# Kernel optimization log

Measured on AMD Instinct MI355X. Metric: run time of the kernel, lower is better.

The kernel has to match this reference:

```python
import jax, jax.numpy as jnp
import numpy as np

B, S, H, F, E, K = 2, 1024, 1024, 4096, 8, 2
TOPK_RATIO = 0.55
EPS = 1e-8


def _ste(x, q):
    # straight-through estimator: forward = q, backward = identity on x
    return x + jax.lax.stop_gradient(q - x)


def ternary_weight(w):
    # BitNet b1.58 absmean ternarization: W -> clip(round(W/mean|W|), -1, 1) * mean|W|
    s = jnp.maximum(jnp.mean(jnp.abs(w)), EPS)
    q = jnp.clip(jnp.round(w / s), -1.0, 1.0) * s
    return _ste(w, q)


def quant_act_int4(x):
    # per-token symmetric int4 fake-quant (range [-7, 7]) with STE
    s = jnp.maximum(jnp.max(jnp.abs(x), axis=-1, keepdims=True), EPS) / 7.0
    q = jnp.clip(jnp.round(x / s), -7.0, 7.0) * s
    return _ste(x, q)


def quant_act_topk_int8(x, ratio):
    # keep top ceil(ratio*d) values by magnitude per token, then int8 fake-quant
    d = x.shape[-1]
    k = int(np.ceil(ratio * d))
    thresh = jax.lax.top_k(jnp.abs(x), k)[0][..., -1:]
    xm = jnp.where(jnp.abs(x) >= thresh, x, 0.0)
    s = jnp.maximum(jnp.max(jnp.abs(xm), axis=-1, keepdims=True), EPS) / 127.0
    q = jnp.clip(jnp.round(xm / s), -127.0, 127.0) * s
    return _ste(xm, q)


def quant_weight_int8(w):
    # per-tensor absmax int8 fake-quant for the router (Int8Linear) with STE
    s = jnp.maximum(jnp.max(jnp.abs(w)), EPS) / 127.0
    q = jnp.clip(jnp.round(w / s), -127.0, 127.0) * s
    return _ste(w, q)


def setup_inputs() -> dict:
    key = jax.random.key(0)
    ks = jax.random.split(key, 5)
    x = jax.random.normal(ks[0], (B, S, H), jnp.float32)
    w_gate = jax.random.normal(ks[1], (E, F, H), jnp.float32) * 0.02
    w_up = jax.random.normal(ks[2], (E, F, H), jnp.float32) * 0.02
    w_down = jax.random.normal(ks[3], (E, H, F), jnp.float32) * 0.02
    w_router = jax.random.normal(ks[4], (E, H), jnp.float32) * 0.02
    return {"x": x, "w_gate": w_gate, "w_up": w_up, "w_down": w_down, "w_router": w_router}


def reference(x, w_gate, w_up, w_down, w_router):
    T = B * S
    xf = x.reshape(T, H)

    # --- router (Int8Linear, higher precision than ternary) ---
    logits = xf @ quant_weight_int8(w_router).T          # [T, E]
    probs = jax.nn.softmax(logits, axis=-1)
    gates, idx = jax.lax.top_k(probs, K)                  # [T, K]
    gates = gates / jnp.sum(gates, axis=-1, keepdims=True)
    # dense combine weights [T, E]
    comb = jnp.zeros((T, E), x.dtype).at[jnp.arange(T)[:, None], idx].set(gates)

    # --- experts: BitFFN (SwiGLU with ternary weights + quantized activations) ---
    xq = quant_act_int4(xf)                               # shared int4 input quant

    def expert(wg, wu, wd):
        g = xq @ ternary_weight(wg).T                     # [T, F]
        u = xq @ ternary_weight(wu).T                     # [T, F]
        h = jax.nn.silu(g) * u
        hq = quant_act_topk_int8(h, TOPK_RATIO)
        return hq @ ternary_weight(wd).T                  # [T, H]

    expert_out = jax.vmap(expert)(w_gate, w_up, w_down)   # [E, T, H]
    out = jnp.einsum('te,eth->th', comb, expert_out)      # gated combine
    return out.reshape(B, S, H)
```

## Files before the change

### kernel.cpp

```cpp
#include <hip/hip_runtime.h>
#include <cstdint>
#include <cstddef>


#define T_TOK 2048
#define HDIM  1024
#define FDIM  4096
#define NEXP  8
#define FH    (FDIM * HDIM)
#define KTOP  2253
#define EPSF  1e-8f
#define PPAD  4608

typedef int v4i  __attribute__((ext_vector_type(4)));
typedef int v16i __attribute__((ext_vector_type(16)));

__global__ __launch_bounds__(256) void k_wabs_partial(const float* __restrict__ wg,
                                                      const float* __restrict__ wu,
                                                      const float* __restrict__ wd,
                                                      float* __restrict__ partials) {
  int m = blockIdx.x, blk = blockIdx.y, tid = threadIdx.x;
  const float* base = (m < 8) ? (wg + (size_t)m * FH)
                    : (m < 16) ? (wu + (size_t)(m - 8) * FH)
                               : (wd + (size_t)(m - 16) * FH);
  size_t start = (size_t)blk * 65536;
  float s = 0.f;
#pragma unroll 4
  for (int i = 0; i < 64; i++) {
    float4 v = *(const float4*)(base + start + (size_t)i * 1024 + tid * 4);
    s += fabsf(v.x) + fabsf(v.y) + fabsf(v.z) + fabsf(v.w);
  }
  for (int o = 32; o > 0; o >>= 1) s += __shfl_down(s, o);
  __shared__ float lds[4];
  if ((tid & 63) == 0) lds[tid >> 6] = s;
  __syncthreads();
  if (tid == 0) partials[m * 64 + blk] = lds[0] + lds[1] + lds[2] + lds[3];
}

__global__ __launch_bounds__(256) void k_scales(const float* __restrict__ wr,
                                                const float* __restrict__ partials,
                                                float* __restrict__ s_w,
                                                float* __restrict__ wrq) {
  int tid = threadIdx.x;
  __shared__ float lds[4];
  __shared__ float sbc;
  for (int m = 0; m < 24; m++) {
    float v = 0.f;
    if (tid < 64) v = partials[m * 64 + tid];
    for (int o = 32; o > 0; o >>= 1) v += __shfl_down(v, o);
    if ((tid & 63) == 0) lds[tid >> 6] = v;
    __syncthreads();
    if (tid == 0) s_w[m] = fmaxf((lds[0] + lds[1] + lds[2] + lds[3]) / (float)FH, EPSF);
    __syncthreads();
  }
  float mx = 0.f;
  for (int i = tid; i < NEXP * HDIM; i += 256) mx = fmaxf(mx, fabsf(wr[i]));
  for (int o = 32; o > 0; o >>= 1) mx = fmaxf(mx, __shfl_down(mx, o));
  if ((tid & 63) == 0) lds[tid >> 6] = mx;
  __syncthreads();
  if (tid == 0)
    sbc = fmaxf(fmaxf(fmaxf(lds[0], lds[1]), fmaxf(lds[2], lds[3])), EPSF) / 127.0f;
  __syncthreads();
  float s = sbc;
  for (int i = tid; i < NEXP * HDIM; i += 256) {
    float q = fminf(fmaxf(rintf(wr[i] / s), -127.f), 127.f);
    wrq[i] = q * s;
  }
}

template <int KD, int RD>
__global__ __launch_bounds__(256) void k_quant_pack(const float* __restrict__ w,
                                                    signed char* __restrict__ q,
                                                    const float* __restrict__ scales) {
  constexpr int CCH = KD / 32, GR = RD / 32;
  int idx = blockIdx.x * 256 + threadIdx.x;
  int l = idx & 63;
  int c = (idx >> 6) % CCH;
  int g = (idx / (64 * CCH)) % GR;
  int e = idx / (64 * CCH * GR);
  const float* src = w + ((size_t)e * RD + g * 32 + (l & 31)) * KD + c * 32 + (l >> 5) * 16;
  float s = scales[e];
  signed char outb[16];
#pragma unroll
  for (int j = 0; j < 4; j++) {
    float4 v = *(const float4*)(src + j * 4);
    outb[j * 4 + 0] = (signed char)(int)fminf(fmaxf(rintf(v.x / s), -1.f), 1.f);
    outb[j * 4 + 1] = (signed char)(int)fminf(fmaxf(rintf(v.y / s), -1.f), 1.f);
    outb[j * 4 + 2] = (signed char)(int)fminf(fmaxf(rintf(v.z / s), -1.f), 1.f);
    outb[j * 4 + 3] = (signed char)(int)fminf(fmaxf(rintf(v.w / s), -1.f), 1.f);
  }
  *(int4*)(q + (size_t)idx * 16) = *(const int4*)outb;
}

__global__ __launch_bounds__(256) void k_act_router(const float* __restrict__ x,
                                                    const float* __restrict__ wrq,
                                                    signed char* __restrict__ xq,
                                                    float* __restrict__ sx,
                                                    int* __restrict__ tok_e,
                                                    float* __restrict__ tok_g,
                                                    int* __restrict__ cnt) {
  int t = blockIdx.x, tid = threadIdx.x;
  float4 xv = *(const float4*)(x + (size_t)t * HDIM + tid * 4);
  __shared__ float lds[4];
  __shared__ float sbc;
  __shared__ float part[8][256];
  __shared__ float lg[8];
  float mx = fmaxf(fmaxf(fabsf(xv.x), fabsf(xv.y)), fmaxf(fabsf(xv.z), fabsf(xv.w)));
  for (int o = 32; o > 0; o >>= 1) mx = fmaxf(mx, __shfl_down(mx, o));
  if ((tid & 63) == 0) lds[tid >> 6] = mx;
  __syncthreads();
  if (tid == 0)
    sbc = fmaxf(fmaxf(fmaxf(lds[0], lds[1]), fmaxf(lds[2], lds[3])), EPSF) / 7.0f;
  __syncthreads();
  float s = sbc;
  int q0 = (int)fminf(fmaxf(rintf(xv.x / s), -7.f), 7.f);
  int q1 = (int)fminf(fmaxf(rintf(xv.y / s), -7.f), 7.f);
  int q2 = (int)fminf(fmaxf(rintf(xv.z / s), -7.f), 7.f);
  int q3 = (int)fminf(fmaxf(rintf(xv.w / s), -7.f), 7.f);
  int packed = (q0 & 255) | ((q1 & 255) << 8) | ((q2 & 255) << 16) | (q3 << 24);
  *(int*)(xq + (size_t)t * HDIM + tid * 4) = packed;
  if (tid == 0) sx[t] = s;
#pragma unroll
  for (int e = 0; e < 8; e++) {
    float4 w = *(const float4*)(wrq + e * HDIM + tid * 4);
    part[e][tid] = xv.x * w.x + xv.y * w.y + xv.z * w.z + xv.w * w.w;
  }
  __syncthreads();
  if (tid < 8) {
    float sum = 0.f;
    for (int i = 0; i < 256; i++) sum += part[tid][i];
    lg[tid] = sum;
  }
  __syncthreads();
  if (tid == 0) {
    float m = lg[0];
    for (int e = 1; e < 8; e++) m = fmaxf(m, lg[e]);
    float p[8]; float S = 0.f;
    for (int e = 0; e < 8; e++) { p[e] = expf(lg[e] - m); S += p[e]; }
    for (int e = 0; e < 8; e++) p[e] /= S;
    int e0 = 0;
    for (int e = 1; e < 8; e++) if (p[e] > p[e0]) e0 = e;
    int e1 = -1;
    for (int e = 0; e < 8; e++) { if (e == e0) continue; if (e1 < 0 || p[e] > p[e1]) e1 = e; }
    float g0 = p[e0], g1 = p[e1], gs = g0 + g1;
    tok_e[2 * t] = e0;  tok_e[2 * t + 1] = e1;
    tok_g[2 * t] = g0 / gs;  tok_g[2 * t + 1] = g1 / gs;
    atomicAdd(&cnt[e0], 1); atomicAdd(&cnt[e1], 1);
  }
}

__global__ void k_plan(const int* __restrict__ cnt, int* __restrict__ offs,
                       int* __restrict__ tile_e, int* __restrict__ tile_m0,
                       int* __restrict__ tile_cnt) {
  if (threadIdx.x == 0 && blockIdx.x == 0) {
    int o = 0;
    for (int e = 0; e < 8; e++) { offs[e] = o; o += (cnt[e] + 63) & ~63; }
    offs[8] = o;
    int tt = 0;
    for (int e = 0; e < 8; e++)
      for (int m0 = 0; m0 < cnt[e]; m0 += 64) { tile_e[tt] = e; tile_m0[tt] = m0; tt++; }
    *tile_cnt = tt;
  }
}

__global__ __launch_bounds__(256) void k_scatter(const int* __restrict__ tok_e,
                                                 const float* __restrict__ tok_g,
                                                 const float* __restrict__ sx,
                                                 const int* __restrict__ offs,
                                                 int* __restrict__ cnt2,
                                                 int* __restrict__ pair_tok,
                                                 float* __restrict__ pair_gate,
                                                 float* __restrict__ pair_sx) {
  int t = blockIdx.x * 256 + threadIdx.x;
  if (t >= T_TOK) return;
  for (int k = 0; k < 2; k++) {
    int e = tok_e[2 * t + k];
    int pos = offs[e] + atomicAdd(&cnt2[e], 1);
    pair_tok[pos] = t;
    pair_gate[pos] = tok_g[2 * t + k];
    pair_sx[pos] = sx[t];
  }
}

__global__ __launch_bounds__(256) void k_packA(const int* __restrict__ pair_tok,
                                               const signed char* __restrict__ xq,
                                               signed char* __restrict__ xqp) {
  int idx = blockIdx.x * 256 + threadIdx.x;
  int l = idx & 63, c = (idx >> 6) & 31, pgrp = idx >> 11;
  int p = pgrp * 32 + (l & 31);
  int tok = pair_tok[p];
  const signed char* src = xq + (size_t)tok * HDIM + c * 32 + (l >> 5) * 16;
  *(int4*)(xqp + (size_t)idx * 16) = *(const int4*)src;
}

__global__ __launch_bounds__(256) void k_gemm_gu(const signed char* __restrict__ xqp,
                                                 const signed char* __restrict__ wgp,
                                                 const signed char* __restrict__ wup,
                                                 const int* __restrict__ tile_e,
                                                 const int* __restrict__ tile_m0,
                                                 const int* __restrict__ tile_cnt,
                                                 const int* __restrict__ cnt,
                                                 const int* __restrict__ offs,
                                                 const float* __restrict__ pair_sx,
                                                 const float* __restrict__ s_w,
                                                 unsigned short* __restrict__ hbuf) {
  int bx = blockIdx.x;
  if (bx >= *tile_cnt) return;
  int e = tile_e[bx], m0 = tile_m0[bx];
  int cnt_e = cnt[e], pbase = offs[e];
  int tid = threadIdx.x;
  int wave = tid >> 6, lane = tid & 63, ln = lane & 31, kh = lane >> 5;
  int fgrp = blockIdx.y * 4 + wave;
  const signed char* bg = wgp + (((size_t)e * 128 + fgrp) * 32) * 1024 + lane * 16;
  const signed char* bu = wup + (((size_t)e * 128 + fgrp) * 32) * 1024 + lane * 16;
  const signed char* ap = xqp + ((size_t)((pbase + m0) >> 5) * 32) * 1024 + lane * 16;
  v16i accg0 = {0}, accg1 = {0}, accu0 = {0}, accu1 = {0};
#pragma unroll 8
  for (int c = 0; c < 32; c++) {
    v4i a0 = *(const v4i*)(ap + c * 1024);
    v4i a1 = *(const v4i*)(ap + 32768 + c * 1024);
    v4i b0 = *(const v4i*)(bg + c * 1024);
    v4i b1 = *(const v4i*)(bu + c * 1024);
    accg0 = __builtin_amdgcn_mfma_i32_32x32x32_i8(a0, b0, accg0, 0, 0, 0);
    accg1 = __builtin_amdgcn_mfma_i32_32x32x32_i8(a1, b0, accg1, 0, 0, 0);
    accu0 = __builtin_amdgcn_mfma_i32_32x32x32_i8(a0, b1, accu0, 0, 0, 0);
    accu1 = __builtin_amdgcn_mfma_i32_32x32x32_i8(a1, b1, accu1, 0, 0, 0);
  }
  float sg = s_w[e], su = s_w[8 + e];
  int col = blockIdx.y * 128 + wave * 32 + ln;
#pragma unroll
  for (int r = 0; r < 16; r++) {
    int rr = (r & 3) + 8 * (r >> 2) + 4 * kh;
#pragma unroll
    for (int mt = 0; mt < 2; mt++) {
      int ml = m0 + mt * 32 + rr;
      if (ml < cnt_e) {
        int p = pbase + ml;
        float sxv = pair_sx[p];
        int gi = (mt == 0) ? accg0[r] : accg1[r];
        int ui = (mt == 0) ? accu0[r] : accu1[r];
        float gf = (float)gi * (sxv * sg);
        float uf = (float)ui * (sxv * su);
        float h = gf / (1.0f + expf(-gf)) * uf;
        ((_Float16*)hbuf)[(size_t)p * FDIM + col] = (_Float16)h;
      }
    }
  }
}

__global__ __launch_bounds__(256) void k_select(const unsigned short* __restrict__ hbuf,
                                                signed char* __restrict__ hqp,
                                                const float* __restrict__ pair_gate,
                                                float* __restrict__ pair_f) {
  int wv = threadIdx.x >> 6, lane = threadIdx.x & 63;
  int p = blockIdx.x * 4 + wv;
  const unsigned short* row = hbuf + (size_t)p * FDIM + lane * 64;
  unsigned short hs[64];
#pragma unroll
  for (int i = 0; i < 8; i++)
    *(uint4*)(hs + i * 8) = *(const uint4*)(row + i * 8);
  unsigned int ua[64];
  unsigned int mxb = 0;
#pragma unroll
  for (int j = 0; j < 64; j++) {
    float v = (float)(((const _Float16*)hs)[j]);
    unsigned int u = __float_as_uint(v) & 0x7fffffffu;
    ua[j] = u;
    mxb = (u > mxb) ? u : mxb;
  }
  for (int o = 32; o > 0; o >>= 1) {
    unsigned int t = (unsigned int)__shfl_down((int)mxb, o);
    mxb = (t > mxb) ? t : mxb;
  }
  mxb = (unsigned int)__shfl((int)mxb, 0);
  unsigned int lo = 0, hi = 0x80000000u;
  for (int it = 0; it < 31; ++it) {
    unsigned int mid = (lo + hi) >> 1;
    int cnt = 0;
#pragma unroll
    for (int j = 0; j < 64; j++)
      cnt += (int)__popcll(__ballot(ua[j] >= mid));
    if (cnt >= KTOP) lo = mid; else hi = mid;
  }
  unsigned int thr = lo;
  float smax = fmaxf(__uint_as_float(mxb), EPSF);
  float sq = smax / 127.0f;
  int pgrp = p >> 5, ln = p & 31;
#pragma unroll
  for (int gj = 0; gj < 4; gj++) {
    int c = 2 * lane + (gj >> 1);
    int kh = gj & 1;
    signed char outb[16];
#pragma unroll
    for (int t = 0; t < 16; t++) {
      int j = gj * 16 + t;
      float v = (float)(((const _Float16*)hs)[j]);
      float m = (ua[j] >= thr) ? v : 0.0f;
      float q = fminf(fmaxf(rintf(m / sq), -127.f), 127.f);
      outb[t] = (signed char)(int)q;
    }
    *(int4*)(hqp + ((size_t)((size_t)pgrp * 128 + c) * 64 + kh * 32 + ln) * 16) =
        *(const int4*)outb;
  }
  if (lane == 0) pair_f[p] = pair_gate[p] * sq;
}

__global__ __launch_bounds__(256) void k_gemm_down(const signed char* __restrict__ hqp,
                                                   const signed char* __restrict__ wdp,
                                                   const int* __restrict__ tile_e,
                                                   const int* __restrict__ tile_m0,
                                                   const int* __restrict__ tile_cnt,
                                                   const int* __restrict__ cnt,
                                                   const int* __restrict__ offs,
                                                   const int* __restrict__ pair_tok,
                                                   const float* __restrict__ pair_f,
                                                   const float* __restrict__ s_w,
                                                   float* __restrict__ out) {
  int bx = blockIdx.x;
  if (bx >= *tile_cnt) return;
  int e = tile_e[bx], m0 = tile_m0[bx];
  int cnt_e = cnt[e], pbase = offs[e];
  int tid = threadIdx.x;
  int wave = tid >> 6, lane = tid & 63, ln = lane & 31, kh = lane >> 5;
  int grp_n = blockIdx.y * 4 + wave;
  const signed char* bp = wdp + (((size_t)e * 32 + grp_n) * 128) * 1024 + lane * 16;
  const signed char* ap = hqp + ((size_t)((pbase + m0) >> 5) * 128) * 1024 + lane * 16;
  v16i acc0 = {0}, acc1 = {0};
#pragma unroll 8
  for (int c = 0; c < 128; c++) {
    v4i a0 = *(const v4i*)(ap + (size_t)c * 1024);
    v4i a1 = *(const v4i*)(ap + 131072 + (size_t)c * 1024);
    v4i b  = *(const v4i*)(bp + (size_t)c * 1024);
    acc0 = __builtin_amdgcn_mfma_i32_32x32x32_i8(a0, b, acc0, 0, 0, 0);
    acc1 = __builtin_amdgcn_mfma_i32_32x32x32_i8(a1, b, acc1, 0, 0, 0);
  }
  float sd = s_w[16 + e];
  int col = blockIdx.y * 128 + wave * 32 + ln;
#pragma unroll
  for (int r = 0; r < 16; r++) {
    int rr = (r & 3) + 8 * (r >> 2) + 4 * kh;
#pragma unroll
    for (int mt = 0; mt < 2; mt++) {
      int ml = m0 + mt * 32 + rr;
      if (ml < cnt_e) {
        int p = pbase + ml;
        int ai = (mt == 0) ? acc0[r] : acc1[r];
        float v = (float)ai * (pair_f[p] * sd);
        atomicAdd(out + (size_t)pair_tok[p] * HDIM + col, v);
      }
    }
  }
}

extern "C" void kernel_launch(void* const* d_in, const int* in_sizes, int n_in,
                              void* d_out, int out_size, void* d_ws, size_t ws_size,
                              hipStream_t stream) {
  const float* x  = (const float*)d_in[0];
  const float* wg = (const float*)d_in[1];
  const float* wu = (const float*)d_in[2];
  const float* wd = (const float*)d_in[3];
  const float* wr = (const float*)d_in[4];
  float* out = (float*)d_out;
  char* ws = (char*)d_ws;
  (void)in_sizes; (void)n_in; (void)out_size; (void)ws_size;

  size_t o = 0;
  auto alloc = [&](size_t b) { size_t r = o; o += (b + 255) & ~(size_t)255; return r; };
  float* partials   = (float*)(ws + alloc(24 * 64 * 4));
  float* s_w        = (float*)(ws + alloc(24 * 4));
  float* wrq        = (float*)(ws + alloc((size_t)NEXP * HDIM * 4));
  int*   tok_e      = (int*)  (ws + alloc((size_t)T_TOK * 2 * 4));
  float* tok_g      = (float*)(ws + alloc((size_t)T_TOK * 2 * 4));
  int*   cnt        = (int*)  (ws + alloc(256));
  int*   cnt2       = cnt + 8;
  int*   offs       = (int*)  (ws + alloc(16 * 4));
  int*   tile_e     = (int*)  (ws + alloc(128 * 4));
  int*   tile_m0    = (int*)  (ws + alloc(128 * 4));
  int*   tile_cnt   = (int*)  (ws + alloc(4));
  int*   pair_tok   = (int*)  (ws + alloc((size_t)PPAD * 4));
  float* pair_gate  = (float*)(ws + alloc((size_t)PPAD * 4));
  float* pair_sx    = (float*)(ws + alloc((size_t)PPAD * 4));
  float* pair_f     = (float*)(ws + alloc((size_t)PPAD * 4));
  float* sx         = (float*)(ws + alloc((size_t)T_TOK * 4));
  signed char* xq   = (signed char*)(ws + alloc((size_t)T_TOK * HDIM));
  signed char* xqp  = (signed char*)(ws + alloc((size_t)PPAD * HDIM));
  signed char* wgp  = (signed char*)(ws + alloc((size_t)NEXP * FH));
  signed char* wup  = (signed char*)(ws + alloc((size_t)NEXP * FH));
  signed char* wdp  = (signed char*)(ws + alloc((size_t)NEXP * FH));
  unsigned short* hbuf = (unsigned short*)(ws + alloc((size_t)PPAD * FDIM * 2));
  signed char* hqp  = (signed char*)(ws + alloc((size_t)PPAD * FDIM));

  hipMemsetAsync(cnt, 0, 64, stream);
  hipMemsetAsync(pair_tok, 0, (size_t)PPAD * 4, stream);
  hipMemsetAsync(out, 0, (size_t)T_TOK * HDIM * 4, stream);

  k_wabs_partial<<<dim3(24, 64), 256, 0, stream>>>(wg, wu, wd, partials);
  k_scales<<<1, 256, 0, stream>>>(wr, partials, s_w, wrq);
  k_quant_pack<1024, 4096><<<8192, 256, 0, stream>>>(wg, wgp, s_w);
  k_quant_pack<1024, 4096><<<8192, 256, 0, stream>>>(wu, wup, s_w + 8);
  k_quant_pack<4096, 1024><<<8192, 256, 0, stream>>>(wd, wdp, s_w + 16);
  k_act_router<<<T_TOK, 256, 0, stream>>>(x, wrq, xq, sx, tok_e, tok_g, cnt);
  k_plan<<<1, 64, 0, stream>>>(cnt, offs, tile_e, tile_m0, tile_cnt);
  k_scatter<<<8, 256, 0, stream>>>(tok_e, tok_g, sx, offs, cnt2, pair_tok, pair_gate, pair_sx);
  k_packA<<<PPAD / 4, 256, 0, stream>>>(pair_tok, xq, xqp);
  k_gemm_gu<<<dim3(72, 32), 256, 0, stream>>>(xqp, wgp, wup, tile_e, tile_m0, tile_cnt,
                                              cnt, offs, pair_sx, s_w, hbuf);
  k_select<<<PPAD / 4, 256, 0, stream>>>(hbuf, hqp, pair_gate, pair_f);
  k_gemm_down<<<dim3(72, 8), 256, 0, stream>>>(hqp, wdp, tile_e, tile_m0, tile_cnt,
                                               cnt, offs, pair_tok, pair_f, s_w, out);
}
```

Before: 816.6 us.

## Interleave per-matrix abs-sum and ternary pack for L2 reuse, use LDS-transposed packing

Weight abs-mean reduction and ternary packing now run per matrix (gate, up, down) in sequence, so each packing pass can re-read weights that may still sit in the large cache. The pack kernel replaces per-element division with a precomputed magnitude threshold found by bisection, and transposes through LDS so both global reads and writes are coalesced. The top-k selection bisection now works on fp16 bit patterns, taking 15 iterations instead of 31. The risks are threshold edge cases where round-half-even at exactly 0.5 differs from the original division, and extra launches.

Result: no change. 810.5 us (-0.7%).

```diff
diff --git a/kernel.cpp b/kernel.cpp
--- a/kernel.cpp
+++ b/kernel.cpp
@@ -15,44 +15,62 @@
 typedef int v4i  __attribute__((ext_vector_type(4)));
 typedef int v16i __attribute__((ext_vector_type(16)));
 
-__global__ __launch_bounds__(256) void k_wabs_partial(const float* __restrict__ wg,
-                                                      const float* __restrict__ wu,
-                                                      const float* __restrict__ wd,
-                                                      float* __restrict__ partials) {
+__global__ __launch_bounds__(256) void k_wabs(const float* __restrict__ w,
+                                              float* __restrict__ partials) {
   int m = blockIdx.x, blk = blockIdx.y, tid = threadIdx.x;
-  const float* base = (m < 8) ? (wg + (size_t)m * FH)
-                    : (m < 16) ? (wu + (size_t)(m - 8) * FH)
-                               : (wd + (size_t)(m - 16) * FH);
-  size_t start = (size_t)blk * 65536;
-  float s = 0.f;
-#pragma unroll 4
-  for (int i = 0; i < 64; i++) {
-    float4 v = *(const float4*)(base + start + (size_t)i * 1024 + tid * 4);
-    s += fabsf(v.x) + fabsf(v.y) + fabsf(v.z) + fabsf(v.w);
-  }
+  const float4* p = (const float4*)(w + (size_t)m * FH + (size_t)blk * 32768) + tid;
+  float s0 = 0.f, s1 = 0.f, s2 = 0.f, s3 = 0.f;
+#pragma unroll
+  for (int i = 0; i < 8; i++) {
+    float4 a = p[(4 * i + 0) * 256];
+    float4 b = p[(4 * i + 1) * 256];
+    float4 c = p[(4 * i + 2) * 256];
+    float4 d = p[(4 * i + 3) * 256];
+    s0 += fabsf(a.x) + fabsf(a.y) + fabsf(a.z) + fabsf(a.w);
+    s1 += fabsf(b.x) + fabsf(b.y) + fabsf(b.z) + fabsf(b.w);
+    s2 += fabsf(c.x) + fabsf(c.y) + fabsf(c.z) + fabsf(c.w);
+    s3 += fabsf(d.x) + fabsf(d.y) + fabsf(d.z) + fabsf(d.w);
+  }
+  float s = (s0 + s1) + (s2 + s3);
   for (int o = 32; o > 0; o >>= 1) s += __shfl_down(s, o);
   __shared__ float lds[4];
   if ((tid & 63) == 0) lds[tid >> 6] = s;
   __syncthreads();
-  if (tid == 0) partials[m * 64 + blk] = lds[0] + lds[1] + lds[2] + lds[3];
-}
-
-__global__ __launch_bounds__(256) void k_scales(const float* __restrict__ wr,
-                                                const float* __restrict__ partials,
-                                                float* __restrict__ s_w,
+  if (tid == 0) partials[m * 128 + blk] = lds[0] + lds[1] + lds[2] + lds[3];
+}
+
+__global__ __launch_bounds__(128) void k_scales8(const float* __restrict__ partials,
+                                                 float* __restrict__ s8,
+                                                 float* __restrict__ thr8) {
+  int tid = threadIdx.x;
+  __shared__ float acc[2];
+  __shared__ float svals[8];
+  for (int m = 0; m < 8; m++) {
+    float v = partials[m * 128 + tid];
+    for (int o = 32; o > 0; o >>= 1) v += __shfl_down(v, o);
+    if ((tid & 63) == 0) acc[tid >> 6] = v;
+    __syncthreads();
+    if (tid == 0) svals[m] = fmaxf((acc[0] + acc[1]) / (float)FH, EPSF);
+    __syncthreads();
+  }
+  if (tid < 8) {
+    float s = svals[tid];
+    s8[tid] = s;
+    unsigned int lo = 0u, hi = __float_as_uint(s);
+    for (int it = 0; it < 32; ++it) {
+      unsigned int mid = (lo + hi) >> 1;
+      if (mid == lo) break;
+      if (__uint_as_float(mid) / s <= 0.5f) lo = mid; else hi = mid;
+    }
+    thr8[tid] = __uint_as_float(lo);
+  }
+}
+
+__global__ __launch_bounds__(256) void k_router(const float* __restrict__ wr,
                                                 float* __restrict__ wrq) {
   int tid = threadIdx.x;
   __shared__ float lds[4];
   __shared__ float sbc;
-  for (int m = 0; m < 24; m++) {
-    float v = 0.f;
-    if (tid < 64) v = partials[m * 64 + tid];
-    for (int o = 32; o > 0; o >>= 1) v += __shfl_down(v, o);
-    if ((tid & 63) == 0) lds[tid >> 6] = v;
-    __syncthreads();
-    if (tid == 0) s_w[m] = fmaxf((lds[0] + lds[1] + lds[2] + lds[3]) / (float)FH, EPSF);
-    __syncthreads();
-  }
   float mx = 0.f;
   for (int i = tid; i < NEXP * HDIM; i += 256) mx = fmaxf(mx, fabsf(wr[i]));
   for (int o = 32; o > 0; o >>= 1) mx = fmaxf(mx, __shfl_down(mx, o));
@@ -69,27 +87,33 @@
 }
 
 template <int KD, int RD>
-__global__ __launch_bounds__(256) void k_quant_pack(const float* __restrict__ w,
-                                                    signed char* __restrict__ q,
-                                                    const float* __restrict__ scales) {
-  constexpr int CCH = KD / 32, GR = RD / 32;
-  int idx = blockIdx.x * 256 + threadIdx.x;
-  int l = idx & 63;
-  int c = (idx >> 6) % CCH;
-  int g = (idx / (64 * CCH)) % GR;
-  int e = idx / (64 * CCH * GR);
-  const float* src = w + ((size_t)e * RD + g * 32 + (l & 31)) * KD + c * 32 + (l >> 5) * 16;
-  float s = scales[e];
-  signed char outb[16];
-#pragma unroll
-  for (int j = 0; j < 4; j++) {
-    float4 v = *(const float4*)(src + j * 4);
-    outb[j * 4 + 0] = (signed char)(int)fminf(fmaxf(rintf(v.x / s), -1.f), 1.f);
-    outb[j * 4 + 1] = (signed char)(int)fminf(fmaxf(rintf(v.y / s), -1.f), 1.f);
-    outb[j * 4 + 2] = (signed char)(int)fminf(fmaxf(rintf(v.z / s), -1.f), 1.f);
-    outb[j * 4 + 3] = (signed char)(int)fminf(fmaxf(rintf(v.w / s), -1.f), 1.f);
-  }
-  *(int4*)(q + (size_t)idx * 16) = *(const int4*)outb;
+__global__ __launch_bounds__(256) void k_pack(const float* __restrict__ w,
+                                              signed char* __restrict__ q,
+                                              const float* __restrict__ thr8) {
+  constexpr int GR = RD / 32, CCH = KD / 32;
+  int e = blockIdx.x / GR, g = blockIdx.x % GR, sl = blockIdx.y;
+  float thr = thr8[e];
+  __shared__ unsigned int lds[32][257];
+  int tid = threadIdx.x;
+  const float* wb = w + ((size_t)e * RD + (size_t)g * 32) * KD + (size_t)sl * 1024;
+#pragma unroll 4
+  for (int i = 0; i < 32; i++) {
+    float4 v = *(const float4*)(wb + (size_t)i * KD + tid * 4);
+    unsigned int b0 = (fabsf(v.x) > thr) ? ((__float_as_uint(v.x) >> 31) ? 0xFFu : 1u) : 0u;
+    unsigned int b1 = (fabsf(v.y) > thr) ? ((__float_as_uint(v.y) >> 31) ? 0xFFu : 1u) : 0u;
+    unsigned int b2 = (fabsf(v.z) > thr) ? ((__float_as_uint(v.z) >> 31) ? 0xFFu : 1u) : 0u;
+    unsigned int b3 = (fabsf(v.w) > thr) ? ((__float_as_uint(v.w) >> 31) ? 0xFFu : 1u) : 0u;
+    lds[i][tid] = b0 | (b1 << 8) | (b2 << 16) | (b3 << 24);
+  }
+  __syncthreads();
+  size_t obase = ((size_t)(e * GR + g) * CCH + (size_t)sl * 32) * 1024;
+#pragma unroll
+  for (int i2 = 0; i2 < 8; i2++) {
+    int mI = i2 * 256 + tid;
+    int c = mI >> 6, l2 = mI & 63, ln = l2 & 31, kh = l2 >> 5;
+    uint4 d = *(const uint4*)&lds[ln][c * 8 + kh * 4];
+    *(uint4*)(q + obase + (size_t)c * 1024 + (size_t)l2 * 16) = d;
+  }
 }
 
 __global__ __launch_bounds__(256) void k_act_router(const float* __restrict__ x,
@@ -259,13 +283,12 @@
 #pragma unroll
   for (int i = 0; i < 8; i++)
     *(uint4*)(hs + i * 8) = *(const uint4*)(row + i * 8);
-  unsigned int ua[64];
+  unsigned short ua[64];
   unsigned int mxb = 0;
 #pragma unroll
   for (int j = 0; j < 64; j++) {
-    float v = (float)(((const _Float16*)hs)[j]);
-    unsigned int u = __float_as_uint(v) & 0x7fffffffu;
-    ua[j] = u;
+    unsigned int u = hs[j] & 0x7fffu;
+    ua[j] = (unsigned short)u;
     mxb = (u > mxb) ? u : mxb;
   }
   for (int o = 32; o > 0; o >>= 1) {
@@ -273,18 +296,19 @@
     mxb = (t > mxb) ? t : mxb;
   }
   mxb = (unsigned int)__shfl((int)mxb, 0);
-  unsigned int lo = 0, hi = 0x80000000u;
-  for (int it = 0; it < 31; ++it) {
+  unsigned int lo = 0, hi = 0x7c00u;
+  for (int it = 0; it < 15; ++it) {
     unsigned int mid = (lo + hi) >> 1;
     int cnt = 0;
 #pragma unroll
     for (int j = 0; j < 64; j++)
-      cnt += (int)__popcll(__ballot(ua[j] >= mid));
+      cnt += (int)__popcll(__ballot((unsigned int)ua[j] >= mid));
     if (cnt >= KTOP) lo = mid; else hi = mid;
   }
   unsigned int thr = lo;
-  float smax = fmaxf(__uint_as_float(mxb), EPSF);
-  float sq = smax / 127.0f;
+  unsigned short mxs = (unsigned short)mxb;
+  float smax = (float)(*(const _Float16*)&mxs);
+  float sq = fmaxf(smax, EPSF) / 127.0f;
   int pgrp = p >> 5, ln = p & 31;
 #pragma unroll
   for (int gj = 0; gj < 4; gj++) {
@@ -295,7 +319,7 @@
     for (int t = 0; t < 16; t++) {
       int j = gj * 16 + t;
       float v = (float)(((const _Float16*)hs)[j]);
-      float m = (ua[j] >= thr) ? v : 0.0f;
+      float m = ((unsigned int)ua[j] >= thr) ? v : 0.0f;
       float q = fminf(fmaxf(rintf(m / sq), -127.f), 127.f);
       outb[t] = (signed char)(int)q;
     }
@@ -366,8 +390,9 @@
 
   size_t o = 0;
   auto alloc = [&](size_t b) { size_t r = o; o += (b + 255) & ~(size_t)255; return r; };
-  float* partials   = (float*)(ws + alloc(24 * 64 * 4));
+  float* partials   = (float*)(ws + alloc(3 * 8 * 128 * 4));
   float* s_w        = (float*)(ws + alloc(24 * 4));
+  float* thr_w      = (float*)(ws + alloc(24 * 4));
   float* wrq        = (float*)(ws + alloc((size_t)NEXP * HDIM * 4));
   int*   tok_e      = (int*)  (ws + alloc((size_t)T_TOK * 2 * 4));
   float* tok_g      = (float*)(ws + alloc((size_t)T_TOK * 2 * 4));
@@ -394,11 +419,19 @@
   hipMemsetAsync(pair_tok, 0, (size_t)PPAD * 4, stream);
   hipMemsetAsync(out, 0, (size_t)T_TOK * HDIM * 4, stream);
 
-  k_wabs_partial<<<dim3(24, 64), 256, 0, stream>>>(wg, wu, wd, partials);
-  k_scales<<<1, 256, 0, stream>>>(wr, partials, s_w, wrq);
-  k_quant_pack<1024, 4096><<<8192, 256, 0, stream>>>(wg, wgp, s_w);
-  k_quant_pack<1024, 4096><<<8192, 256, 0, stream>>>(wu, wup, s_w + 8);
-  k_quant_pack<4096, 1024><<<8192, 256, 0, stream>>>(wd, wdp, s_w + 16);
+  k_wabs<<<dim3(8, 128), 256, 0, stream>>>(wg, partials);
+  k_scales8<<<1, 128, 0, stream>>>(partials, s_w, thr_w);
+  k_pack<1024, 4096><<<dim3(1024, 1), 256, 0, stream>>>(wg, wgp, thr_w);
+
+  k_wabs<<<dim3(8, 128), 256, 0, stream>>>(wu, partials + 1024);
+  k_scales8<<<1, 128, 0, stream>>>(partials + 1024, s_w + 8, thr_w + 8);
+  k_pack<1024, 4096><<<dim3(1024, 1), 256, 0, stream>>>(wu, wup, thr_w + 8);
+
+  k_wabs<<<dim3(8, 128), 256, 0, stream>>>(wd, partials + 2048);
+  k_scales8<<<1, 128, 0, stream>>>(partials + 2048, s_w + 16, thr_w + 16);
+  k_pack<4096, 1024><<<dim3(256, 4), 256, 0, stream>>>(wd, wdp, thr_w + 16);
+
+  k_router<<<1, 256, 0, stream>>>(wr, wrq);
   k_act_router<<<T_TOK, 256, 0, stream>>>(x, wrq, xq, sx, tok_e, tok_g, cnt);
   k_plan<<<1, 64, 0, stream>>>(cnt, offs, tile_e, tile_m0, tile_cnt);
   k_scatter<<<8, 256, 0, stream>>>(tok_e, tok_g, sx, offs, cnt2, pair_tok, pair_gate, pair_sx);
```
